# Kernel tuning notes

Hardware: AMD Instinct MI355X
Metric: run time of the kernel (lower is better)

The kernel has to match this reference:

```python
import jax, jax.numpy as jnp
import numpy as np

B, C, L = 32, 128, 4096
TIME_DIM = 512
K_TOP = 8


def setup_inputs() -> dict:
    key = jax.random.key(0)
    k1, k2, k3, k4 = jax.random.split(key, 4)
    x = jax.random.normal(k1, (B, C, L), dtype=jnp.float32)
    time_emb = jax.random.normal(k2, (B, TIME_DIM), dtype=jnp.float32)
    # nn.Linear(time_dim, channels): weight (C, time_dim), bias (C,)
    W = jax.random.normal(k3, (C, TIME_DIM), dtype=jnp.float32) / np.sqrt(TIME_DIM)
    b = jax.random.normal(k4, (C,), dtype=jnp.float32) * 0.01
    return {"x": x, "time_emb": time_emb, "W": W, "b": b}


def reference(x, time_emb, W, b):
    Bn, Cn, n = x.shape
    k = min(K_TOP, n // 2 + 1)
    # time-conditioned modulation: Linear -> tanh -> (1 + tanh) scale
    scale = time_emb @ W.T + b                      # (B, C)
    x_mod = x * (1.0 + jnp.tanh(scale))[:, :, None]  # (B, C, L)
    # rFFT along time
    x_fft = jnp.fft.rfft(x_mod, axis=-1)             # (B, C, F) complex64
    amp = jnp.abs(x_fft)
    # top-k frequency bins per (b, c) row
    _, topk_idx = jax.lax.top_k(amp, k)              # (B, C, k)
    gathered = jnp.take_along_axis(x_fft, topk_idx, axis=-1)
    bi = jnp.arange(Bn)[:, None, None]
    ci = jnp.arange(Cn)[None, :, None]
    masked_fft = jnp.zeros_like(x_fft).at[bi, ci, topk_idx].set(gathered)
    p_it = jnp.fft.irfft(masked_fft, n=n, axis=-1)
    return p_it.astype(x.dtype)
```

## Files before the change

kernel.cpp:

```cpp
#include <hip/hip_runtime.h>

#define LL 4096
#define THREADS 512
#define KK 8

typedef float v2f __attribute__((ext_vector_type(2)));

#define PD(i) ((i) + ((i) >> 4))
#define PERM8(r) ((((r) & 3) << 1) | ((r) >> 2))

__device__ __forceinline__ float sinr(float x) {
    float r; asm("v_sin_f32 %0, %1" : "=v"(r) : "v"(x)); return r;
}
__device__ __forceinline__ float cosr(float x) {
    float r; asm("v_cos_f32 %0, %1" : "=v"(r) : "v"(x)); return r;
}

__device__ __forceinline__ v2f padd(v2f a, v2f b) {
    v2f d; asm("v_pk_add_f32 %0, %1, %2" : "=v"(d) : "v"(a), "v"(b)); return d;
}
__device__ __forceinline__ v2f psub(v2f a, v2f b) {
    v2f d; asm("v_pk_add_f32 %0, %1, %2 neg_lo:[0,1] neg_hi:[0,1]" : "=v"(d) : "v"(a), "v"(b)); return d;
}
__device__ __forceinline__ v2f addmi(v2f a, v2f b) {
    v2f d; asm("v_pk_add_f32 %0, %1, %2 op_sel:[0,1] op_sel_hi:[1,0] neg_hi:[0,1]" : "=v"(d) : "v"(a), "v"(b)); return d;
}
__device__ __forceinline__ v2f submi(v2f a, v2f b) {
    v2f d; asm("v_pk_add_f32 %0, %1, %2 op_sel:[0,1] op_sel_hi:[1,0] neg_lo:[0,1]" : "=v"(d) : "v"(a), "v"(b)); return d;
}
__device__ __forceinline__ v2f negi(v2f a) {
    v2f d; asm("v_pk_add_f32 %0, %1, 0 op_sel:[1,0] op_sel_hi:[0,0] neg_hi:[1,0]" : "=v"(d) : "v"(a)); return d;
}
__device__ __forceinline__ v2f pfma(v2f a, v2f b, v2f c) {
    v2f d; asm("v_pk_fma_f32 %0, %1, %2, %3" : "=v"(d) : "v"(a), "v"(b), "v"(c)); return d;
}
__device__ __forceinline__ v2f pfms(v2f a, v2f b, v2f c) {
    v2f d; asm("v_pk_fma_f32 %0, %1, %2, %3 neg_lo:[0,0,1] neg_hi:[0,0,1]" : "=v"(d) : "v"(a), "v"(b), "v"(c)); return d;
}
__device__ __forceinline__ v2f cmul(v2f a, v2f b) {
    v2f t, d;
    asm("v_pk_mul_f32 %0, %1, %2 op_sel:[0,0] op_sel_hi:[0,1]" : "=v"(t) : "v"(a), "v"(b));
    asm("v_pk_fma_f32 %0, %1, %2, %3 op_sel:[1,1,0] op_sel_hi:[1,0,1] neg_lo:[1,0,0]"
        : "=v"(d) : "v"(a), "v"(b), "v"(t));
    return d;
}
__device__ __forceinline__ v2f cmulw(v2f z, v2f w) {
    v2f t, d;
    asm("v_pk_mul_f32 %0, %1, %2 op_sel:[0,0] op_sel_hi:[1,0]" : "=v"(t) : "v"(z), "v"(w));
    asm("v_pk_fma_f32 %0, %1, %2, %3 op_sel:[1,1,0] op_sel_hi:[0,1,1] neg_hi:[1,0,0]"
        : "=v"(d) : "v"(z), "v"(w), "v"(t));
    return d;
}
__device__ __forceinline__ v2f unt0(v2f z, v2f y) {
    v2f d; asm("v_pk_add_f32 %0, %1, %2 neg_hi:[0,1]" : "=v"(d) : "v"(z), "v"(y)); return d;
}
__device__ __forceinline__ v2f unt1(v2f z, v2f y) {
    v2f d; asm("v_pk_add_f32 %0, %1, %2 op_sel:[1,1] op_sel_hi:[0,0] neg_hi:[1,0]" : "=v"(d) : "v"(z), "v"(y)); return d;
}

__device__ __forceinline__ void dft4(v2f& a, v2f& b, v2f& c, v2f& d) {
    v2f t0 = padd(a, c), t1 = psub(a, c);
    v2f t2 = padd(b, d), t3 = psub(b, d);
    a = padd(t0, t2); c = psub(t0, t2);
    b = addmi(t1, t3); d = submi(t1, t3);
}

__device__ __forceinline__ void dft8(v2f* v) {
    dft4(v[0], v[2], v[4], v[6]);
    dft4(v[1], v[3], v[5], v[7]);
    const float C2 = 0.70710678118654752f;
    const v2f W81 = (v2f){C2, C2};
    const v2f W83 = (v2f){-C2, C2};
    v[3] = cmulw(v[3], W81);
    v[5] = negi(v[5]);
    v[7] = cmulw(v[7], W83);
#pragma unroll
    for (int k0 = 0; k0 < 4; ++k0) {
        v2f a = v[2 * k0], b = v[2 * k0 + 1];
        v[2 * k0]     = padd(a, b);
        v[2 * k0 + 1] = psub(a, b);
    }
}

__device__ __forceinline__ void twiddle7(v2f* v, float th) {
    v2f w1 = (v2f){cosr(th), sinr(th)};
    v2f w2 = cmul(w1, w1);
    v2f w3 = cmul(w2, w1);
    v2f w4 = cmul(w2, w2);
    v2f w5 = cmul(w3, w2);
    v2f w6 = cmul(w3, w3);
    v2f w7 = cmul(w4, w3);
    v[1] = cmulw(v[1], w1);
    v[2] = cmulw(v[2], w2);
    v[3] = cmulw(v[3], w3);
    v[4] = cmulw(v[4], w4);
    v[5] = cmulw(v[5], w5);
    v[6] = cmulw(v[6], w6);
    v[7] = cmulw(v[7], w7);
}

#define DPP_STEP(CTRL)                                                          \
  {                                                                             \
    int vs_ = __builtin_amdgcn_update_dpp(__float_as_int(bv), __float_as_int(bv), \
                                          CTRL, 0xf, 0xf, false);               \
    int bs_ = __builtin_amdgcn_update_dpp(bb, bb, CTRL, 0xf, 0xf, false);       \
    float vf_ = __int_as_float(vs_);                                            \
    bool tk_ = (vf_ > bv) || (vf_ == bv && bs_ < bb);                           \
    bv = tk_ ? vf_ : bv; bb = tk_ ? bs_ : bb;                                   \
  }

__global__ __launch_bounds__(THREADS, 8)
void fft2_topk_k(const float* __restrict__ x, const float* __restrict__ te,
                 const float* __restrict__ W, const float* __restrict__ bias,
                 float* __restrict__ out) {
    __shared__ v2f zb[4353];
    __shared__ float wv[8];
    __shared__ float candV[2][16];
    __shared__ int   candB[2][16];
    __shared__ v2f  selAB[2][KK];
    __shared__ int  selF[2][KK];
    __shared__ v2f  stepT[16];

    int t = threadIdx.x;
    int pair = blockIdx.x;
    int b = pair >> 6;
    int c0 = (pair & 63) << 1;
    int row0 = (b << 7) + c0;

    {
        int mh = t >> 8, tt = t & 255;
        const float* tp = te + b * 512;
        const float* wp = W + (c0 + mh) * 512;
        float ps = tp[tt] * wp[tt] + tp[tt + 256] * wp[tt + 256];
#pragma unroll
        for (int off = 32; off; off >>= 1) ps += __shfl_down(ps, off);
        if ((t & 63) == 0) wv[t >> 6] = ps;
    }

    const float* xp0 = x + (size_t)row0 * LL;
    const float* xp1 = xp0 + LL;
    v2f v[8];
#pragma unroll
    for (int r = 0; r < 8; ++r) { v[r].x = xp0[t + 512 * r]; v[r].y = xp1[t + 512 * r]; }
    __syncthreads();
    float g0 = 1.0f + tanhf(wv[0] + wv[1] + wv[2] + wv[3] + bias[c0]);
    float g1 = 1.0f + tanhf(wv[4] + wv[5] + wv[6] + wv[7] + bias[c0 + 1]);
    {
        v2f g = (v2f){g0, g1};
#pragma unroll
        for (int r = 0; r < 8; ++r) v[r] *= g;
    }

    dft8(v);
    {
        int wb = 8 * t + (t >> 1);
#pragma unroll
        for (int r = 0; r < 8; ++r) zb[wb + r] = v[PERM8(r)];
    }
    __syncthreads();

    int rb = t + (t >> 4);

#pragma unroll
    for (int r = 0; r < 8; ++r) v[r] = zb[rb + 544 * r];
    twiddle7(v, (float)(t & 7) * (1.0f / 64.0f));
    dft8(v);
    __syncthreads();
    {
        int wb = 64 * (t >> 3) + (t & 7);
        int B0 = wb + (wb >> 4);
        int B1 = (wb + 8) + ((wb + 8) >> 4);
#pragma unroll
        for (int s = 0; s < 4; ++s) {
            zb[B0 + 17 * s] = v[PERM8(2 * s)];
            zb[B1 + 17 * s] = v[PERM8(2 * s + 1)];
        }
    }
    __syncthreads();

#pragma unroll
    for (int r = 0; r < 8; ++r) v[r] = zb[rb + 544 * r];
    twiddle7(v, (float)(t & 63) * (1.0f / 512.0f));
    dft8(v);
    __syncthreads();
    {
        int wb = 512 * (t >> 6) + (t & 63);
        int B2 = wb + (wb >> 4);
#pragma unroll
        for (int r = 0; r < 8; ++r) zb[B2 + 68 * r] = v[PERM8(r)];
    }
    __syncthreads();

#pragma unroll
    for (int r = 0; r < 8; ++r) v[r] = zb[rb + 544 * r];
    twiddle7(v, (float)t * (1.0f / 4096.0f));
    dft8(v);
#pragma unroll
    for (int r = 0; r < 8; ++r) zb[rb + 544 * r] = v[PERM8(r)];
    if (t == 0) zb[4352] = v[0];
    __syncthreads();

    int wid = t >> 6, lane = t & 63;

    if (wid < 4) {
        int row = wid >> 1, hf = wid & 1;
        int kb = (hf << 10) + lane;
        int base1 = PD(kb);
        int base2 = PD(4096 - kb);
        float amp[16];
        float lv = -1.f; int lm = 0;
#pragma unroll
        for (int m = 0; m < 16; ++m) {
            v2f z = zb[base1 + 68 * m];
            v2f y = zb[base2 - 68 * m];
            v2f X = row ? unt1(z, y) : unt0(z, y);
            float a = fmaf(X.x, X.x, X.y * X.y);
            amp[m] = a;
            if (a > lv) { lv = a; lm = m; }
        }
        for (int it = 0; it < KK; ++it) {
            float bv = lv; int bb = kb + (lm << 6);
            DPP_STEP(0x111)
            DPP_STEP(0x112)
            DPP_STEP(0x114)
            DPP_STEP(0x118)
            DPP_STEP(0x142)
            DPP_STEP(0x143)
            float vwin = __int_as_float(__builtin_amdgcn_readlane(__float_as_int(bv), 63));
            int   wbin = __builtin_amdgcn_readlane(bb, 63);
            if (lane == 0) { candV[row][(hf << 3) + it] = vwin; candB[row][(hf << 3) + it] = wbin; }
            if ((wbin & 63) == lane) {
                int m0 = ((wbin - (hf << 10)) >> 6);
                lv = -1.f; lm = 0;
#pragma unroll
                for (int m = 0; m < 16; ++m) {
                    float a = (m == m0) ? -1.f : amp[m];
                    amp[m] = a;
                    if (a > lv) { lv = a; lm = m; }
                }
            }
        }
    }
    __syncthreads();

    if (wid < 2 && lane < 17) {
        int row = wid;
        v2f z2 = zb[PD(2048)];
        float xn = 2.f * (row ? z2.y : z2.x);
        float a2048 = xn * xn;
        float myv; int myb, rank;
        if (lane < 16) {
            myv = candV[row][lane]; myb = candB[row][lane];
            rank = lane & 7;
            int ob = (lane < 8) ? 8 : 0;
#pragma unroll
            for (int j = 0; j < 8; ++j) {
                float ov = candV[row][ob + j]; int obn = candB[row][ob + j];
                if (ov > myv || (ov == myv && obn < myb)) rank++;
            }
            if (a2048 > myv) rank++;
        } else {
            myv = a2048; myb = 2048; rank = 0;
#pragma unroll
            for (int j = 0; j < 16; ++j)
                if (candV[row][j] >= myv) rank++;
        }
        if (rank < KK) {
            v2f z = zb[PD(myb)];
            v2f y = zb[PD(4096 - myb)];
            v2f X;
            if (row == 0) X = (v2f){0.5f * (z.x + y.x), 0.5f * (z.y - y.y)};
            else          X = (v2f){0.5f * (z.y + y.y), 0.5f * (y.x - z.x)};
            bool edge = (myb == 0) || (myb == 2048);
            float wgt = edge ? 1.f : 2.f;
            selF[row][rank] = myb;
            selAB[row][rank] = (v2f){wgt * (1.0f / 4096.0f) * X.x,
                                     edge ? 0.f : wgt * (1.0f / 4096.0f) * X.y};
        }
    }
    if (wid == 4 && lane < 16) {
        float a = (float)lane * (1.0f / 16.0f);
        stepT[lane] = (v2f){cosr(a), sinr(a)};
    }
    __syncthreads();

    {
        int mh = t >> 8, u = t & 255;
        const float i4096 = 1.0f / 4096.0f;
        v2f rc[4], rp[4], tcv[4], sgv[4];
#pragma unroll
        for (int j = 0; j < 4; ++j) {
            int f0 = selF[mh][2 * j], f1 = selF[mh][2 * j + 1];
            v2f A0 = selAB[mh][2 * j], A1 = selAB[mh][2 * j + 1];
            int m0a = (f0 * u) & 4095, m0b = (f1 * u) & 4095;
            float c0a = cosr((float)m0a * i4096), s0a = sinr((float)m0a * i4096);
            float c0b = cosr((float)m0b * i4096), s0b = sinr((float)m0b * i4096);
            float r0a = A0.x * c0a - A0.y * s0a;
            float i0a = A0.x * s0a + A0.y * c0a;
            float r0b = A1.x * c0b - A1.y * s0b;
            float i0b = A1.x * s0b + A1.y * c0b;
            v2f st0 = stepT[f0 & 15];
            v2f st1 = stepT[f1 & 15];
            rc[j] = (v2f){r0a, r0b};
            rp[j] = (v2f){r0a * st0.x + i0a * st0.y, r0b * st1.x + i0b * st1.y};
            tcv[j] = (v2f){st0.x + st0.x, st1.x + st1.x};
            sgv[j] = (v2f){(f0 & 1) ? -1.f : 1.f, (f1 & 1) ? -1.f : 1.f};
        }
        float* op = out + (size_t)(row0 + mh) * LL;
#pragma unroll
        for (int q2 = 0; q2 < 8; ++q2) {
            v2f accv = padd(padd(rc[0], rc[1]), padd(rc[2], rc[3]));
            v2f acdv = pfma(rc[0], sgv[0],
                       pfma(rc[1], sgv[1],
                       pfma(rc[2], sgv[2], rc[3] * sgv[3])));
            op[u + (q2 << 8)] = accv.x + accv.y;
            op[u + (q2 << 8) + 2048] = acdv.x + acdv.y;
#pragma unroll
            for (int j = 0; j < 4; ++j) {
                v2f rn = pfms(tcv[j], rc[j], rp[j]);
                rp[j] = rc[j];
                rc[j] = rn;
            }
        }
    }
}

extern "C" void kernel_launch(void* const* d_in, const int* in_sizes, int n_in,
                              void* d_out, int out_size, void* d_ws, size_t ws_size,
                              hipStream_t stream) {
    const float* x    = (const float*)d_in[0];
    const float* te   = (const float*)d_in[1];
    const float* W    = (const float*)d_in[2];
    const float* bias = (const float*)d_in[3];
    float* out = (float*)d_out;
    fft2_topk_k<<<2048, THREADS, 0, stream>>>(x, te, W, bias, out);
}
```

Baseline: 47.24 us.

## Defer time-scale to selected bins, DPP reduction, and table-based twiddles

The per-row modulation gain is now applied only to the selected top-k coefficients instead of scaling all input samples. Because the gain is a positive per-row constant, the top-k ordering stays the same, and this removes the early __syncthreads that waited on the linear-layer reduction before the FFT. The wave reduction uses DPP row operations instead of shuffles. The per-thread cos/sin evaluations for the inverse synthesis are replaced by lookups in two 64-entry shared tables combined with a complex multiply, which trades transcendental instructions for LDS reads.

```diff
diff --git a/kernel.cpp b/kernel.cpp
--- a/kernel.cpp
+++ b/kernel.cpp
@@ -21,6 +21,9 @@
 }
 __device__ __forceinline__ v2f psub(v2f a, v2f b) {
     v2f d; asm("v_pk_add_f32 %0, %1, %2 neg_lo:[0,1] neg_hi:[0,1]" : "=v"(d) : "v"(a), "v"(b)); return d;
+}
+__device__ __forceinline__ v2f pmul(v2f a, v2f b) {
+    v2f d; asm("v_pk_mul_f32 %0, %1, %2" : "=v"(d) : "v"(a), "v"(b)); return d;
 }
 __device__ __forceinline__ v2f addmi(v2f a, v2f b) {
     v2f d; asm("v_pk_add_f32 %0, %1, %2 op_sel:[0,1] op_sel_hi:[1,0] neg_hi:[0,1]" : "=v"(d) : "v"(a), "v"(b)); return d;
@@ -108,6 +111,9 @@
     bool tk_ = (vf_ > bv) || (vf_ == bv && bs_ < bb);                           \
     bv = tk_ ? vf_ : bv; bb = tk_ ? bs_ : bb;                                   \
   }
+#define DPP_ADD(CTRL)                                                           \
+  ps += __int_as_float(__builtin_amdgcn_update_dpp(0, __float_as_int(ps),       \
+                                                   CTRL, 0xf, 0xf, true));
 
 __global__ __launch_bounds__(THREADS, 8)
 void fft2_topk_k(const float* __restrict__ x, const float* __restrict__ te,
@@ -119,7 +125,7 @@
     __shared__ int   candB[2][16];
     __shared__ v2f  selAB[2][KK];
     __shared__ int  selF[2][KK];
-    __shared__ v2f  stepT[16];
+    __shared__ v2f  T1[64], T2[64];
 
     int t = threadIdx.x;
     int pair = blockIdx.x;
@@ -132,9 +138,16 @@
         const float* tp = te + b * 512;
         const float* wp = W + (c0 + mh) * 512;
         float ps = tp[tt] * wp[tt] + tp[tt + 256] * wp[tt + 256];
-#pragma unroll
-        for (int off = 32; off; off >>= 1) ps += __shfl_down(ps, off);
-        if ((t & 63) == 0) wv[t >> 6] = ps;
+        DPP_ADD(0x111) DPP_ADD(0x112) DPP_ADD(0x114) DPP_ADD(0x118)
+        DPP_ADD(0x142) DPP_ADD(0x143)
+        if ((t & 63) == 63) wv[t >> 6] = ps;
+    }
+    if (t < 64) {
+        float a = (float)t * (1.0f / 64.0f);
+        T1[t] = (v2f){cosr(a), sinr(a)};
+    } else if (t < 128) {
+        float a = (float)(t - 64) * (1.0f / 4096.0f);
+        T2[t - 64] = (v2f){cosr(a), sinr(a)};
     }
 
     const float* xp0 = x + (size_t)row0 * LL;
@@ -142,14 +155,6 @@
     v2f v[8];
 #pragma unroll
     for (int r = 0; r < 8; ++r) { v[r].x = xp0[t + 512 * r]; v[r].y = xp1[t + 512 * r]; }
-    __syncthreads();
-    float g0 = 1.0f + tanhf(wv[0] + wv[1] + wv[2] + wv[3] + bias[c0]);
-    float g1 = 1.0f + tanhf(wv[4] + wv[5] + wv[6] + wv[7] + bias[c0 + 1]);
-    {
-        v2f g = (v2f){g0, g1};
-#pragma unroll
-        for (int r = 0; r < 8; ++r) v[r] *= g;
-    }
 
     dft8(v);
     {
@@ -245,6 +250,8 @@
 
     if (wid < 2 && lane < 17) {
         int row = wid;
+        float g = 1.0f + tanhf(wv[4 * row] + wv[4 * row + 1] + wv[4 * row + 2]
+                               + wv[4 * row + 3] + bias[c0 + row]);
         v2f z2 = zb[PD(2048)];
         float xn = 2.f * (row ? z2.y : z2.x);
         float a2048 = xn * xn;
@@ -272,38 +279,30 @@
             if (row == 0) X = (v2f){0.5f * (z.x + y.x), 0.5f * (z.y - y.y)};
             else          X = (v2f){0.5f * (z.y + y.y), 0.5f * (y.x - z.x)};
             bool edge = (myb == 0) || (myb == 2048);
-            float wgt = edge ? 1.f : 2.f;
+            float wgt = (edge ? 1.f : 2.f) * g * (1.0f / 4096.0f);
             selF[row][rank] = myb;
-            selAB[row][rank] = (v2f){wgt * (1.0f / 4096.0f) * X.x,
-                                     edge ? 0.f : wgt * (1.0f / 4096.0f) * X.y};
-        }
-    }
-    if (wid == 4 && lane < 16) {
-        float a = (float)lane * (1.0f / 16.0f);
-        stepT[lane] = (v2f){cosr(a), sinr(a)};
+            selAB[row][rank] = (v2f){wgt * X.x, edge ? 0.f : wgt * X.y};
+        }
     }
     __syncthreads();
 
     {
         int mh = t >> 8, u = t & 255;
-        const float i4096 = 1.0f / 4096.0f;
         v2f rc[4], rp[4], tcv[4], sgv[4];
 #pragma unroll
         for (int j = 0; j < 4; ++j) {
             int f0 = selF[mh][2 * j], f1 = selF[mh][2 * j + 1];
             v2f A0 = selAB[mh][2 * j], A1 = selAB[mh][2 * j + 1];
-            int m0a = (f0 * u) & 4095, m0b = (f1 * u) & 4095;
-            float c0a = cosr((float)m0a * i4096), s0a = sinr((float)m0a * i4096);
-            float c0b = cosr((float)m0b * i4096), s0b = sinr((float)m0b * i4096);
-            float r0a = A0.x * c0a - A0.y * s0a;
-            float i0a = A0.x * s0a + A0.y * c0a;
-            float r0b = A1.x * c0b - A1.y * s0b;
-            float i0b = A1.x * s0b + A1.y * c0b;
-            v2f st0 = stepT[f0 & 15];
-            v2f st1 = stepT[f1 & 15];
-            rc[j] = (v2f){r0a, r0b};
-            rp[j] = (v2f){r0a * st0.x + i0a * st0.y, r0b * st1.x + i0b * st1.y};
-            tcv[j] = (v2f){st0.x + st0.x, st1.x + st1.x};
+            int m0 = (f0 * u) & 4095, m1 = (f1 * u) & 4095;
+            v2f e0 = cmul(T1[m0 >> 6], T2[m0 & 63]);
+            v2f e1 = cmul(T1[m1 >> 6], T2[m1 & 63]);
+            v2f w0 = cmul(A0, e0);
+            v2f w1 = cmul(A1, e1);
+            v2f s0 = T1[(f0 & 15) << 2];
+            v2f s1 = T1[(f1 & 15) << 2];
+            rc[j] = (v2f){w0.x, w1.x};
+            rp[j] = (v2f){w0.x * s0.x + w0.y * s0.y, w1.x * s1.x + w1.y * s1.y};
+            tcv[j] = (v2f){s0.x + s0.x, s1.x + s1.x};
             sgv[j] = (v2f){(f0 & 1) ? -1.f : 1.f, (f1 & 1) ? -1.f : 1.f};
         }
         float* op = out + (size_t)(row0 + mh) * LL;
@@ -312,7 +311,7 @@
             v2f accv = padd(padd(rc[0], rc[1]), padd(rc[2], rc[3]));
             v2f acdv = pfma(rc[0], sgv[0],
                        pfma(rc[1], sgv[1],
-                       pfma(rc[2], sgv[2], rc[3] * sgv[3])));
+                       pfma(rc[2], sgv[2], pmul(rc[3], sgv[3]))));
             op[u + (q2 << 8)] = accv.x + accv.y;
             op[u + (q2 << 8) + 2048] = acdv.x + acdv.y;
 #pragma unroll
```

Result: no change. 46.77 us (-1.0%).
